# Optimization experiments

Measured on AMD Instinct MI355X. Metric: run time of the kernel, lower is better.

The kernel has to match this reference:

```python
import jax, jax.numpy as jnp
import numpy as np


def segment_softmax(x, seg, num_segments):
    # numerically-stable softmax over graph segments (rows of the sparse matrix)
    m = jax.ops.segment_max(x, seg, num_segments=num_segments)
    e = jnp.exp(x - m[seg])
    s = jax.ops.segment_sum(e, seg, num_segments=num_segments)
    return e / s[seg]


def setup_inputs() -> dict:
    key = jax.random.key(0)
    ks = jax.random.split(key, 12)
    B, N, E, P, H = 256, 51200, 102400, 5, 300
    instruction = jax.random.normal(ks[0], (B, H), dtype=jnp.float32)
    distribution = jax.random.uniform(ks[1], (N,), dtype=jnp.float32)
    node_attrs = jax.random.normal(ks[2], (N, H), dtype=jnp.float32)
    edge_attrs = jax.random.normal(ks[3], (E, H), dtype=jnp.float32)
    node_indices = jnp.sort(jax.random.randint(ks[4], (N,), 0, B)).astype(jnp.int32)
    edge_batch_indices = jax.random.randint(ks[5], (E,), 0, B).astype(jnp.int32)
    edge_indices = jax.random.randint(ks[6], (2, E), 0, N).astype(jnp.int32)
    prop_embeds = jax.random.normal(ks[7], (P, H), dtype=jnp.float32)
    Ws_property = jax.random.uniform(ks[8], (P, H, H), dtype=jnp.float32)
    W_state = jax.random.uniform(ks[9], (H,), dtype=jnp.float32)
    W_relation = jax.random.uniform(ks[10], (H,), dtype=jnp.float32)
    return {"instruction": instruction, "distribution": distribution, "node_attrs": node_attrs,
            "edge_attrs": edge_attrs, "node_indices": node_indices,
            "edge_batch_indices": edge_batch_indices, "edge_indices": edge_indices,
            "prop_embeds": prop_embeds, "Ws_property": Ws_property,
            "W_state": W_state, "W_relation": W_relation}


def reference(instruction, distribution, node_attrs, edge_attrs, node_indices,
              edge_batch_indices, edge_indices, prop_embeds, Ws_property,
              W_state, W_relation):
    B = instruction.shape[0]
    # [B, P] property similarities
    prop_sim = jax.nn.softmax(instruction @ prop_embeds.T, axis=1)
    ps_node = prop_sim[node_indices]            # [N, P]
    instr_node = instruction[node_indices]      # [N, H]
    # per-property transform of node attrs: [N, P-1, H]
    wx = jnp.einsum('phk,nk->nph', Ws_property[:-1], node_attrs)
    node_scores = jax.nn.elu(jnp.sum(ps_node[:, :-1, None] * instr_node[:, None, :] * wx, axis=1))  # [N, H]
    # relation transform of edge attrs: [E, H]
    edge_wx = jnp.einsum('hk,ek->eh', Ws_property[-1], edge_attrs)
    edge_scores = jax.nn.elu(instruction[edge_batch_indices] * edge_wx)  # [E, H]
    # per-graph (segment) softmax over state logits
    state_logits = node_scores @ W_state        # [N]
    next_states = segment_softmax(state_logits, node_indices, B)
    # scatter-add message passing: dst node accumulates distribution[src] * edge_scores
    agg = jnp.zeros_like(node_scores).at[edge_indices[1]].add(
        distribution[edge_indices[0], None] * edge_scores)  # [N, H]
    rel_logits = agg @ W_relation               # [N]
    next_relations = segment_softmax(rel_logits, node_indices, B)
    r = ps_node[:, -1]
    next_distribution = r * next_relations + (1.0 - r) * next_states
    return next_distribution, prop_sim
```

## Files before the change

### kernel.cpp

```cpp
#include <hip/hip_runtime.h>
#include <math.h>

#define H 300
#define PP 5
#define NE 128
#define KC 32
#define NCH 10
#define ROWB 128
#define WTILE (320 * ROWB)
#define WHALF (160 * ROWB)
#define ATILE (NE * ROWB)
#define NTHREADS 256
#define GT 512

using short8 = __attribute__((ext_vector_type(8))) short;
using f32x4  = __attribute__((ext_vector_type(4))) float;

__device__ __forceinline__ float wsum64(float v) {
#pragma unroll
    for (int m = 32; m >= 1; m >>= 1) v += __shfl_xor(v, m, 64);
    return v;
}
__device__ __forceinline__ float wmax64(float v) {
#pragma unroll
    for (int m = 32; m >= 1; m >>= 1) v = fmaxf(v, __shfl_xor(v, m, 64));
    return v;
}
__device__ __forceinline__ float eluf(float x) { return x > 0.f ? x : expm1f(x); }

__device__ __forceinline__ unsigned short f2bf(float x) {
    unsigned int u = __float_as_uint(x);
    unsigned int r = u + 0x7FFF + ((u >> 16) & 1);
    return (unsigned short)(r >> 16);
}
__device__ __forceinline__ float bf2f(unsigned short h) {
    return __uint_as_float(((unsigned int)h) << 16);
}
__device__ __forceinline__ int sw(int r, int kb) {
    return r * ROWB + (kb ^ ((r & 7) << 4));
}
__device__ __forceinline__ void split4(const float* v, uint2& ph, uint2& pl) {
    unsigned short hs[4], ls[4];
#pragma unroll
    for (int i = 0; i < 4; ++i) {
        hs[i] = f2bf(v[i]);
        ls[i] = f2bf(v[i] - bf2f(hs[i]));
    }
    ph = make_uint2((unsigned)hs[0] | ((unsigned)hs[1] << 16),
                    (unsigned)hs[2] | ((unsigned)hs[3] << 16));
    pl = make_uint2((unsigned)ls[0] | ((unsigned)ls[1] << 16),
                    (unsigned)ls[2] | ((unsigned)ls[3] << 16));
}
__device__ __forceinline__ void gload16(const void* g, void* lds) {
    __builtin_amdgcn_global_load_lds(
        (const __attribute__((address_space(1))) unsigned int*)g,
        (__attribute__((address_space(3))) unsigned int*)lds, 16, 0, 0);
}
#define SBAR() __builtin_amdgcn_s_barrier()
#define SCHED() __builtin_amdgcn_sched_barrier(0)
#define WAIT_LGKM() asm volatile("s_waitcnt lgkmcnt(0)" ::: "memory")
#define WAIT_VM0()  asm volatile("s_waitcnt vmcnt(0)" ::: "memory")
#define WAIT_VM4()  asm volatile("s_waitcnt vmcnt(4)" ::: "memory")
#define WAIT_VM5()  asm volatile("s_waitcnt vmcnt(5)" ::: "memory")

__global__ void k_prop_sim(const float* __restrict__ instr,
                           const float* __restrict__ pe,
                           float* __restrict__ prop_sim) {
    int b = blockIdx.x, lane = threadIdx.x;
    float dots[PP];
#pragma unroll
    for (int p = 0; p < PP; ++p) {
        float s = 0.f;
        for (int hh = lane; hh < H; hh += 64) s += instr[b * H + hh] * pe[p * H + hh];
        dots[p] = wsum64(s);
    }
    if (lane == 0) {
        float m = dots[0];
#pragma unroll
        for (int p = 1; p < PP; ++p) m = fmaxf(m, dots[p]);
        float e[PP], s = 0.f;
#pragma unroll
        for (int p = 0; p < PP; ++p) { e[p] = expf(dots[p] - m); s += e[p]; }
        float inv = 1.f / s;
#pragma unroll
        for (int p = 0; p < PP; ++p) prop_sim[b * PP + p] = e[p] * inv;
    }
}

__global__ void k_counts(const int* __restrict__ idx, int* __restrict__ counts, int N) {
    int i = blockIdx.x * blockDim.x + threadIdx.x;
    if (i < N) atomicAdd(&counts[idx[i]], 1);
}

__global__ void k_scan(const int* __restrict__ counts, int* __restrict__ offsets, int B) {
    __shared__ int sh[256];
    int t = threadIdx.x;
    int c = (t < B) ? counts[t] : 0;
    sh[t] = c;
    __syncthreads();
    for (int off = 1; off < 256; off <<= 1) {
        int v = (t >= off) ? sh[t - off] : 0;
        __syncthreads();
        sh[t] += v;
        __syncthreads();
    }
    if (t < B) offsets[t] = sh[t] - c;
    if (t == B - 1) offsets[B] = sh[t];
}

__global__ void k_presplit(const float* __restrict__ W4, char* __restrict__ img) {
    int c = blockIdx.x;
    int idx = blockIdx.y * NTHREADS + threadIdx.x;
    int r = idx >> 3, j = idx & 7;
    int k = c * KC + j * 4;
    float v[4] = {0.f, 0.f, 0.f, 0.f};
    if (r < H && k < H) *(float4*)v = *(const float4*)&W4[(size_t)r * H + k];
    uint2 ph, pl;
    split4(v, ph, pl);
    char* row = img + (size_t)c * WTILE + (size_t)r * ROWB;
    int x = (r & 7) << 4;
    *(uint2*)(row + ((j * 8) ^ x)) = ph;
    *(uint2*)(row + ((64 + j * 8) ^ x)) = pl;
}

__global__ void k_combine(const float* __restrict__ Ws,
                          const float* __restrict__ prop_sim,
                          char* __restrict__ img) {
    int b = blockIdx.x, c = blockIdx.y, t = threadIdx.x;
    float ps0 = prop_sim[b * PP + 0], ps1 = prop_sim[b * PP + 1];
    float ps2 = prop_sim[b * PP + 2], ps3 = prop_sim[b * PP + 3];
    char* tile = img + ((size_t)b * NCH + c) * WTILE;
#pragma unroll
    for (int i = 0; i < 10; ++i) {
        int idx = t + i * NTHREADS;
        int r = idx >> 3, j = idx & 7;
        int k = c * KC + j * 4;
        float cv[4] = {0.f, 0.f, 0.f, 0.f};
        if (r < H && k < H) {
            size_t base = (size_t)r * H + k;
            float w0[4], w1[4], w2[4], w3[4];
            *(float4*)w0 = *(const float4*)&Ws[0 * (size_t)H * H + base];
            *(float4*)w1 = *(const float4*)&Ws[1 * (size_t)H * H + base];
            *(float4*)w2 = *(const float4*)&Ws[2 * (size_t)H * H + base];
            *(float4*)w3 = *(const float4*)&Ws[3 * (size_t)H * H + base];
#pragma unroll
            for (int q = 0; q < 4; ++q)
                cv[q] = fmaf(ps0, w0[q], fmaf(ps1, w1[q], fmaf(ps2, w2[q], ps3 * w3[q])));
        }
        uint2 ph, pl;
        split4(cv, ph, pl);
        char* row = tile + (size_t)r * ROWB;
        int x = (r & 7) << 4;
        *(uint2*)(row + ((j * 8) ^ x)) = ph;
        *(uint2*)(row + ((64 + j * 8) ^ x)) = pl;
    }
}

__global__ __launch_bounds__(GT, 2) void k_gemm(
    const float* __restrict__ na, const float* __restrict__ ea,
    const char* __restrict__ Wc_img, const char* __restrict__ Wr_img,
    const float* __restrict__ instr, const float* __restrict__ wstate,
    const float* __restrict__ wrel,
    const int* __restrict__ offsets, const int* __restrict__ eb,
    const int* __restrict__ ei, const float* __restrict__ dist,
    float* __restrict__ slog, float* __restrict__ rlog,
    int N, int E, int nodeBlks)
{
    __shared__ __align__(16) char W_t[2][WHALF];
    __shared__ __align__(16) char A_t[ATILE];

    int bid = blockIdx.x;
    int hz = blockIdx.y;
    bool isNode = bid < nodeBlks;
    const float* Asrc;
    const char* Wsrc;
    int base, rowmax, b = 0, nn = NE;
    if (isNode) {
        int low3 = bid & 7, q = bid >> 3;
        int tile = q % 3, bhi = q / 3;
        b = bhi * 8 + low3;
        int start = offsets[b], end = offsets[b + 1];
        base = start + tile * NE;
        if (base >= end) return;
        nn = min(NE, end - base);
        rowmax = N - 1;
        Asrc = na;
        Wsrc = Wc_img + (size_t)b * NCH * WTILE + (size_t)hz * WHALF;
    } else {
        base = (bid - nodeBlks) * NE;
        rowmax = E - 1;
        Asrc = ea;
        Wsrc = Wr_img + (size_t)hz * WHALF;
    }

    int t = threadIdx.x;
    int w = t >> 6, l = t & 63, lane16 = l & 15, g = l >> 4;
    int wn = w & 3, wh = w >> 2;

    f32x4 acc[5][2];
#pragma unroll
    for (int ht = 0; ht < 5; ++ht)
#pragma unroll
        for (int cg = 0; cg < 2; ++cg) acc[ht][cg] = (f32x4){0.f, 0.f, 0.f, 0.f};

    float4 pa[2];

    auto loadA = [&](int c) {
#pragma unroll
        for (int i = 0; i < 2; ++i) {
            int idx = t + i * GT;
            int r = idx >> 3, j = idx & 7;
            int k = c * KC + j * 4;
            float4 v = {0.f, 0.f, 0.f, 0.f};
            if (k < H) {
                int row = min(base + r, rowmax);
                v = *(const float4*)&Asrc[(size_t)row * H + k];
            }
            pa[i] = v;
        }
    };
    auto storeA = [&]() {
#pragma unroll
        for (int i = 0; i < 2; ++i) {
            int idx = t + i * GT;
            int r = idx >> 3, j = idx & 7;
            float v[4] = {pa[i].x, pa[i].y, pa[i].z, pa[i].w};
            uint2 ph, pl;
            split4(v, ph, pl);
            *(uint2*)(A_t + sw(r, j * 8)) = ph;
            *(uint2*)(A_t + sw(r, 64 + j * 8)) = pl;
        }
    };
    auto gloadW = [&](int c, int sel) {
        const char* src = Wsrc + (size_t)c * WTILE;
        char* dst = W_t[sel];
        int off = w * 1024 + (l << 4);
        gload16(src + off, dst + off);
        gload16(src + 8192 + off, dst + 8192 + off);
        if (w < 4) gload16(src + 16384 + off, dst + 16384 + off);
    };

    loadA(0);
    gloadW(0, 0);
    storeA();
    loadA(1);
    gloadW(1, 1);
    SCHED();
    if (w < 4) { WAIT_VM5(); } else { WAIT_VM4(); }
    WAIT_LGKM();
    SBAR();
    SCHED();

    int curb = 0;
    for (int c = 0; c < NCH; ++c) {
        short8 bh[2], bl[2];
#pragma unroll
        for (int cg = 0; cg < 2; ++cg) {
            int brow = wn * 32 + cg * 16 + lane16;
            bh[cg] = *(const short8*)(A_t + sw(brow, g * 16));
            bl[cg] = *(const short8*)(A_t + sw(brow, 64 + g * 16));
        }
#pragma unroll
        for (int ht = 0; ht < 5; ++ht) {
            int arow = wh * 80 + ht * 16 + lane16;
            short8 ah = *(const short8*)(W_t[curb] + sw(arow, g * 16));
            short8 al = *(const short8*)(W_t[curb] + sw(arow, 64 + g * 16));
#pragma unroll
            for (int cg = 0; cg < 2; ++cg) {
                acc[ht][cg] = __builtin_amdgcn_mfma_f32_16x16x32_bf16(ah, bh[cg], acc[ht][cg], 0, 0, 0);
                acc[ht][cg] = __builtin_amdgcn_mfma_f32_16x16x32_bf16(ah, bl[cg], acc[ht][cg], 0, 0, 0);
                acc[ht][cg] = __builtin_amdgcn_mfma_f32_16x16x32_bf16(al, bh[cg], acc[ht][cg], 0, 0, 0);
            }
        }
        if (c + 1 < NCH) {
            WAIT_LGKM();
            SBAR();
            SCHED();
            storeA();
            if (c + 2 < NCH) {
                loadA(c + 2);
                gloadW(c + 2, curb);
                SCHED();
                if (w < 4) { WAIT_VM5(); } else { WAIT_VM4(); }
            } else {
                SCHED();
                WAIT_VM0();
            }
            WAIT_LGKM();
            SBAR();
            SCHED();
            curb ^= 1;
        }
    }

    if (isNode) {
        const float* insb = instr + (size_t)b * H;
#pragma unroll
        for (int cg = 0; cg < 2; ++cg) {
            float part = 0.f;
#pragma unroll
            for (int ht = 0; ht < 5; ++ht) {
                int hb = hz * 160 + wh * 80 + ht * 16 + g * 4;
#pragma unroll
                for (int r = 0; r < 4; ++r) {
                    int h = hb + r;
                    if (h < H) part += wstate[h] * eluf(insb[h] * acc[ht][cg][r]);
                }
            }
            part += __shfl_xor(part, 16, 64);
            part += __shfl_xor(part, 32, 64);
            int col = wn * 32 + cg * 16 + lane16;
            if (l < 16 && col < nn) atomicAdd(&slog[base + col], part);
        }
    } else {
#pragma unroll
        for (int cg = 0; cg < 2; ++cg) {
            int e = base + wn * 32 + cg * 16 + lane16;
            int be = eb[e];
            const float* insb = instr + (size_t)be * H;
            float part = 0.f;
#pragma unroll
            for (int ht = 0; ht < 5; ++ht) {
                int hb = hz * 160 + wh * 80 + ht * 16 + g * 4;
#pragma unroll
                for (int r = 0; r < 4; ++r) {
                    int h = hb + r;
                    if (h < H) part += wrel[h] * eluf(insb[h] * acc[ht][cg][r]);
                }
            }
            part += __shfl_xor(part, 16, 64);
            part += __shfl_xor(part, 32, 64);
            if (l < 16) atomicAdd(&rlog[ei[E + e]], dist[ei[e]] * part);
        }
    }
}

__global__ void k_final(const float* __restrict__ slog, const float* __restrict__ rlog,
                        const float* __restrict__ prop_sim, const int* __restrict__ offsets,
                        float* __restrict__ out)
{
    int b = blockIdx.x;
    int s0 = offsets[b], e1 = offsets[b + 1];
    int t = threadIdx.x, wave = t >> 6, lane = t & 63;
    __shared__ float shA[4], shB[4];
    float mS = -3.0e38f, mR = -3.0e38f;
    for (int i = s0 + t; i < e1; i += 256) {
        mS = fmaxf(mS, slog[i]);
        mR = fmaxf(mR, rlog[i]);
    }
    mS = wmax64(mS); mR = wmax64(mR);
    if (lane == 0) { shA[wave] = mS; shB[wave] = mR; }
    __syncthreads();
    mS = fmaxf(fmaxf(shA[0], shA[1]), fmaxf(shA[2], shA[3]));
    mR = fmaxf(fmaxf(shB[0], shB[1]), fmaxf(shB[2], shB[3]));
    __syncthreads();
    float sS = 0.f, sR = 0.f;
    for (int i = s0 + t; i < e1; i += 256) {
        sS += expf(slog[i] - mS);
        sR += expf(rlog[i] - mR);
    }
    sS = wsum64(sS); sR = wsum64(sR);
    if (lane == 0) { shA[wave] = sS; shB[wave] = sR; }
    __syncthreads();
    sS = shA[0] + shA[1] + shA[2] + shA[3];
    sR = shB[0] + shB[1] + shB[2] + shB[3];
    float r = prop_sim[b * PP + (PP - 1)];
    float iS = 1.f / sS, iR = 1.f / sR;
    for (int i = s0 + t; i < e1; i += 256) {
        float ns = expf(slog[i] - mS) * iS;
        float nr = expf(rlog[i] - mR) * iR;
        out[i] = r * nr + (1.f - r) * ns;
    }
}

extern "C" void kernel_launch(void* const* d_in, const int* in_sizes, int n_in,
                              void* d_out, int out_size, void* d_ws, size_t ws_size,
                              hipStream_t stream) {
    (void)n_in; (void)out_size; (void)ws_size;
    const float* instruction  = (const float*)d_in[0];
    const float* distribution = (const float*)d_in[1];
    const float* node_attrs   = (const float*)d_in[2];
    const float* edge_attrs   = (const float*)d_in[3];
    const int*   node_indices = (const int*)d_in[4];
    const int*   edge_batch   = (const int*)d_in[5];
    const int*   edge_indices = (const int*)d_in[6];
    const float* prop_embeds  = (const float*)d_in[7];
    const float* Ws           = (const float*)d_in[8];
    const float* W_state      = (const float*)d_in[9];
    const float* W_rel        = (const float*)d_in[10];

    int B = in_sizes[0] / H;
    int N = in_sizes[1];
    int E = in_sizes[5];

    float* out = (float*)d_out;
    float* prop_sim = out + N;

    float* ws = (float*)d_ws;
    float* state_logits = ws;
    float* rel_logits   = ws + N;
    int*   offsets      = (int*)(ws + 2 * (size_t)N);
    int*   counts       = offsets + (B + 1);
    uintptr_t wsp = (uintptr_t)(counts + B);
    wsp = (wsp + 255) & ~(uintptr_t)255;
    char* Wr_img = (char*)wsp;
    char* Wc_img = Wr_img + (size_t)NCH * WTILE;

    size_t zero_bytes = (size_t)2 * N * sizeof(float) + (size_t)(2 * B + 1) * sizeof(int);
    hipMemsetAsync(d_ws, 0, zero_bytes, stream);

    int nodeBlks = 3 * B;
    int edgeBlks = E / NE;

    k_prop_sim<<<B, 64, 0, stream>>>(instruction, prop_embeds, prop_sim);
    k_presplit<<<dim3(NCH, 10), NTHREADS, 0, stream>>>(Ws + 4 * (size_t)H * H, Wr_img);
    k_counts<<<(N + 255) / 256, 256, 0, stream>>>(node_indices, counts, N);
    k_scan<<<1, 256, 0, stream>>>(counts, offsets, B);
    k_combine<<<dim3(B, NCH), NTHREADS, 0, stream>>>(Ws, prop_sim, Wc_img);
    k_gemm<<<dim3(nodeBlks + edgeBlks, 2), GT, 0, stream>>>(
        node_attrs, edge_attrs, Wc_img, Wr_img, instruction, W_state, W_rel,
        offsets, edge_batch, edge_indices, distribution,
        state_logits, rel_logits, N, E, nodeBlks);
    k_final<<<B, 256, 0, stream>>>(state_logits, rel_logits, prop_sim, offsets, out);
}
```

Before: 337.9 us.

## Fold instruction scale into combined weights, remap grid, split MFMA loop with setprio

Three separate changes. The per-batch instruction vector is multiplied into the combined weight image ahead of time, so the node epilogue no longer loads instr and multiplies per element. The 2D grid becomes a 1D grid whose index mapping interleaves the two H halves and the tiles of each batch group, which changes block ordering and cache locality for the weight image. The inner MFMA loop is split into two phases that load the LDS operands first and then raise wave priority around the MFMA bursts, aiming for better overlap of LDS reads and matrix math across waves. The bf16 split of the pre-scaled weights may change rounding slightly.

```diff
diff --git a/kernel.cpp b/kernel.cpp
--- a/kernel.cpp
+++ b/kernel.cpp
@@ -125,6 +125,7 @@
 
 __global__ void k_combine(const float* __restrict__ Ws,
                           const float* __restrict__ prop_sim,
+                          const float* __restrict__ instr,
                           char* __restrict__ img) {
     int b = blockIdx.x, c = blockIdx.y, t = threadIdx.x;
     float ps0 = prop_sim[b * PP + 0], ps1 = prop_sim[b * PP + 1];
@@ -137,6 +138,7 @@
         int k = c * KC + j * 4;
         float cv[4] = {0.f, 0.f, 0.f, 0.f};
         if (r < H && k < H) {
+            float insv = instr[(size_t)b * H + r];
             size_t base = (size_t)r * H + k;
             float w0[4], w1[4], w2[4], w3[4];
             *(float4*)w0 = *(const float4*)&Ws[0 * (size_t)H * H + base];
@@ -145,7 +147,7 @@
             *(float4*)w3 = *(const float4*)&Ws[3 * (size_t)H * H + base];
 #pragma unroll
             for (int q = 0; q < 4; ++q)
-                cv[q] = fmaf(ps0, w0[q], fmaf(ps1, w1[q], fmaf(ps2, w2[q], ps3 * w3[q])));
+                cv[q] = insv * fmaf(ps0, w0[q], fmaf(ps1, w1[q], fmaf(ps2, w2[q], ps3 * w3[q])));
         }
         uint2 ph, pl;
         split4(cv, ph, pl);
@@ -164,21 +166,22 @@
     const int* __restrict__ offsets, const int* __restrict__ eb,
     const int* __restrict__ ei, const float* __restrict__ dist,
     float* __restrict__ slog, float* __restrict__ rlog,
-    int N, int E, int nodeBlks)
+    int N, int E, int nodeVX)
 {
     __shared__ __align__(16) char W_t[2][WHALF];
     __shared__ __align__(16) char A_t[ATILE];
 
-    int bid = blockIdx.x;
-    int hz = blockIdx.y;
-    bool isNode = bid < nodeBlks;
+    int x = blockIdx.x;
+    bool isNode = x < nodeVX;
     const float* Asrc;
     const char* Wsrc;
-    int base, rowmax, b = 0, nn = NE;
+    int base, rowmax, b = 0, hz, nn = NE;
     if (isNode) {
-        int low3 = bid & 7, q = bid >> 3;
-        int tile = q % 3, bhi = q / 3;
-        b = bhi * 8 + low3;
+        int g = x / 48, r = x - g * 48;
+        int k = r >> 3;
+        b = g * 8 + (r & 7);
+        int tile = k >> 1;
+        hz = k & 1;
         int start = offsets[b], end = offsets[b + 1];
         base = start + tile * NE;
         if (base >= end) return;
@@ -187,7 +190,11 @@
         Asrc = na;
         Wsrc = Wc_img + (size_t)b * NCH * WTILE + (size_t)hz * WHALF;
     } else {
-        base = (bid - nodeBlks) * NE;
+        int y = x - nodeVX;
+        int g = y / 16, r = y - g * 16;
+        int e = g * 8 + (r & 7);
+        hz = r >> 3;
+        base = e * NE;
         rowmax = E - 1;
         Asrc = ea;
         Wsrc = Wr_img + (size_t)hz * WHALF;
@@ -260,17 +267,47 @@
             bh[cg] = *(const short8*)(A_t + sw(brow, g * 16));
             bl[cg] = *(const short8*)(A_t + sw(brow, 64 + g * 16));
         }
-#pragma unroll
-        for (int ht = 0; ht < 5; ++ht) {
-            int arow = wh * 80 + ht * 16 + lane16;
-            short8 ah = *(const short8*)(W_t[curb] + sw(arow, g * 16));
-            short8 al = *(const short8*)(W_t[curb] + sw(arow, 64 + g * 16));
-#pragma unroll
-            for (int cg = 0; cg < 2; ++cg) {
-                acc[ht][cg] = __builtin_amdgcn_mfma_f32_16x16x32_bf16(ah, bh[cg], acc[ht][cg], 0, 0, 0);
-                acc[ht][cg] = __builtin_amdgcn_mfma_f32_16x16x32_bf16(ah, bl[cg], acc[ht][cg], 0, 0, 0);
-                acc[ht][cg] = __builtin_amdgcn_mfma_f32_16x16x32_bf16(al, bh[cg], acc[ht][cg], 0, 0, 0);
-            }
+        {
+            short8 ah[2], al[2];
+#pragma unroll
+            for (int ht = 0; ht < 2; ++ht) {
+                int arow = wh * 80 + ht * 16 + lane16;
+                ah[ht] = *(const short8*)(W_t[curb] + sw(arow, g * 16));
+                al[ht] = *(const short8*)(W_t[curb] + sw(arow, 64 + g * 16));
+            }
+            SCHED();
+            __builtin_amdgcn_s_setprio(1);
+#pragma unroll
+            for (int ht = 0; ht < 2; ++ht)
+#pragma unroll
+                for (int cg = 0; cg < 2; ++cg) {
+                    acc[ht][cg] = __builtin_amdgcn_mfma_f32_16x16x32_bf16(ah[ht], bh[cg], acc[ht][cg], 0, 0, 0);
+                    acc[ht][cg] = __builtin_amdgcn_mfma_f32_16x16x32_bf16(ah[ht], bl[cg], acc[ht][cg], 0, 0, 0);
+                    acc[ht][cg] = __builtin_amdgcn_mfma_f32_16x16x32_bf16(al[ht], bh[cg], acc[ht][cg], 0, 0, 0);
+                }
+            __builtin_amdgcn_s_setprio(0);
+            SCHED();
+        }
+        {
+            short8 ah[3], al[3];
+#pragma unroll
+            for (int ht = 0; ht < 3; ++ht) {
+                int arow = wh * 80 + (ht + 2) * 16 + lane16;
+                ah[ht] = *(const short8*)(W_t[curb] + sw(arow, g * 16));
+                al[ht] = *(const short8*)(W_t[curb] + sw(arow, 64 + g * 16));
+            }
+            SCHED();
+            __builtin_amdgcn_s_setprio(1);
+#pragma unroll
+            for (int ht = 0; ht < 3; ++ht)
+#pragma unroll
+                for (int cg = 0; cg < 2; ++cg) {
+                    acc[ht + 2][cg] = __builtin_amdgcn_mfma_f32_16x16x32_bf16(ah[ht], bh[cg], acc[ht + 2][cg], 0, 0, 0);
+                    acc[ht + 2][cg] = __builtin_amdgcn_mfma_f32_16x16x32_bf16(ah[ht], bl[cg], acc[ht + 2][cg], 0, 0, 0);
+                    acc[ht + 2][cg] = __builtin_amdgcn_mfma_f32_16x16x32_bf16(al[ht], bh[cg], acc[ht + 2][cg], 0, 0, 0);
+                }
+            __builtin_amdgcn_s_setprio(0);
+            SCHED();
         }
         if (c + 1 < NCH) {
             WAIT_LGKM();
@@ -294,7 +331,6 @@
     }
 
     if (isNode) {
-        const float* insb = instr + (size_t)b * H;
 #pragma unroll
         for (int cg = 0; cg < 2; ++cg) {
             float part = 0.f;
@@ -304,7 +340,7 @@
 #pragma unroll
                 for (int r = 0; r < 4; ++r) {
                     int h = hb + r;
-                    if (h < H) part += wstate[h] * eluf(insb[h] * acc[ht][cg][r]);
+                    if (h < H) part += wstate[h] * eluf(acc[ht][cg][r]);
                 }
             }
             part += __shfl_xor(part, 16, 64);
@@ -409,17 +445,17 @@
     size_t zero_bytes = (size_t)2 * N * sizeof(float) + (size_t)(2 * B + 1) * sizeof(int);
     hipMemsetAsync(d_ws, 0, zero_bytes, stream);
 
-    int nodeBlks = 3 * B;
-    int edgeBlks = E / NE;
+    int nodeVX = 6 * B;
+    int edgeVX = (E / NE) * 2;
 
     k_prop_sim<<<B, 64, 0, stream>>>(instruction, prop_embeds, prop_sim);
     k_presplit<<<dim3(NCH, 10), NTHREADS, 0, stream>>>(Ws + 4 * (size_t)H * H, Wr_img);
     k_counts<<<(N + 255) / 256, 256, 0, stream>>>(node_indices, counts, N);
     k_scan<<<1, 256, 0, stream>>>(counts, offsets, B);
-    k_combine<<<dim3(B, NCH), NTHREADS, 0, stream>>>(Ws, prop_sim, Wc_img);
-    k_gemm<<<dim3(nodeBlks + edgeBlks, 2), GT, 0, stream>>>(
+    k_combine<<<dim3(B, NCH), NTHREADS, 0, stream>>>(Ws, prop_sim, instruction, Wc_img);
+    k_gemm<<<nodeVX + edgeVX, GT, 0, stream>>>(
         node_attrs, edge_attrs, Wc_img, Wr_img, instruction, W_state, W_rel,
         offsets, edge_batch, edge_indices, distribution,
-        state_logits, rel_logits, N, E, nodeBlks);
+        state_logits, rel_logits, N, E, nodeVX);
     k_final<<<B, 256, 0, stream>>>(state_logits, rel_logits, prop_sim, offsets, out);
 }
```

Result: slower. 390.9 us (+15.7%).
